# Performance work log

Hardware: AMD Instinct MI355X
Metric: run time of the kernel (lower is better)

The kernel has to match this reference:

```python
import jax, jax.numpy as jnp
import numpy as np

P = 2            # power (even positive int)
TEMPERATURE = 1.0
SCALE = 1.0 / np.sqrt(64.0)  # sqrt(head_dim) scaling
EPS = 1e-6


def setup_inputs() -> dict:
    key = jax.random.key(0)
    kq, kk, kv = jax.random.split(key, 3)
    shape = (4, 16, 2048, 64)  # (B, H, N, head_dim)
    return {
        "q": jax.random.normal(kq, shape, dtype=jnp.float32),
        "k": jax.random.normal(kk, shape, dtype=jnp.float32),
        "v": jax.random.normal(kv, shape, dtype=jnp.float32),
    }


def reference(q, k, v):
    # logits = q @ k^T * scale / temperature : (B, H, N, N)
    logits = jnp.einsum("bhnd,bhmd->bhnm", q, k) * (SCALE / TEMPERATURE)
    attn = logits ** P
    attn = attn / (attn.sum(axis=-1, keepdims=True) + EPS)
    return jnp.einsum("bhnm,bhmd->bhnd", attn, v)
```

## Files before the change

### kernel.cpp

```cpp
#include <hip/hip_runtime.h>

#define N_CTX 2048
#define DHEAD 64
#define SCALE_F 0.125f
#define EPS_F 1e-6f
#define KT 64
#define NITER (N_CTX / KT)
#define QBLK 256

typedef __attribute__((ext_vector_type(8))) short short8;
typedef __attribute__((ext_vector_type(4))) short short4v;
typedef __attribute__((ext_vector_type(4))) float float4v;
typedef __attribute__((ext_vector_type(2))) unsigned uint2v;
typedef __attribute__((ext_vector_type(4))) unsigned uint4v;

#if defined(__HIP_DEVICE_COMPILE__) && __has_builtin(__builtin_amdgcn_cvt_pk_bf16_f32)
typedef __attribute__((ext_vector_type(2))) __bf16 bf16x2;
__device__ __forceinline__ unsigned pack2(float a, float b) {
    union { bf16x2 v; unsigned u; } x;
    x.v = __builtin_amdgcn_cvt_pk_bf16_f32(a, b);
    return x.u;
}
#else
__device__ __forceinline__ unsigned bf1(float f) {
    union { float f; unsigned u; } x; x.f = f;
    return (x.u + 0x7FFFu + ((x.u >> 16) & 1u)) >> 16;
}
__device__ __forceinline__ unsigned pack2(float a, float b) {
    return bf1(a) | (bf1(b) << 16);
}
#endif

#if defined(__HIP_DEVICE_COMPILE__)
  #if __has_builtin(__builtin_amdgcn_mfma_f32_16x16x16bf16_1k)
    #define MFMA16(a, b, c) __builtin_amdgcn_mfma_f32_16x16x16bf16_1k(a, b, c, 0, 0, 0)
  #elif __has_builtin(__builtin_amdgcn_mfma_f32_16x16x16_bf16_1k)
    #define MFMA16(a, b, c) __builtin_amdgcn_mfma_f32_16x16x16_bf16_1k(a, b, c, 0, 0, 0)
  #else
    __device__ __forceinline__ float4v mfma16_asm(short4v a, short4v b, float4v c) {
        asm volatile("v_mfma_f32_16x16x16_bf16 %0, %1, %2, %0"
                     : "+v"(c) : "v"(a), "v"(b));
        return c;
    }
    #define MFMA16(a, b, c) mfma16_asm(a, b, c)
  #endif
#else
  #define MFMA16(a, b, c) (c)
#endif


__global__ __launch_bounds__(256, 2)
void powsm_attn(const float* __restrict__ qg, const float* __restrict__ kg,
                const float* __restrict__ vg, float* __restrict__ og)
{
    __shared__ short Ks[64][72];
    __shared__ short Vt[64][68];
    __shared__ float Dn[4][64];

    const int bh   = blockIdx.y;
    const int tid  = threadIdx.x;
    const int wave = tid >> 6;
    const int lane = tid & 63;
    const int qd   = lane >> 4;
    const int c    = lane & 15;

    const size_t base = (size_t)bh * N_CTX * DHEAD;
    const float* qp = qg + base;
    const float* kp = kg + base;
    const float* vp = vg + base;
    float*       op = og + base;

    const int qw0 = blockIdx.x * QBLK + wave * 64;

    short8 Qf[4][2];
    #pragma unroll
    for (int qt = 0; qt < 4; ++qt) {
        #pragma unroll
        for (int ks = 0; ks < 2; ++ks) {
            const float* src = qp + (size_t)(qw0 + qt*16 + c) * DHEAD + ks*32 + qd*8;
            float4v a = *(const float4v*)(src);
            float4v b = *(const float4v*)(src + 4);
            uint4v u;
            u[0] = pack2(a[0]*SCALE_F, a[1]*SCALE_F);
            u[1] = pack2(a[2]*SCALE_F, a[3]*SCALE_F);
            u[2] = pack2(b[0]*SCALE_F, b[1]*SCALE_F);
            u[3] = pack2(b[2]*SCALE_F, b[3]*SCALE_F);
            union { uint4v u; short8 s; } cv; cv.u = u;
            Qf[qt][ks] = cv.s;
        }
    }

    float4v Oacc[4][4];
    #pragma unroll
    for (int qt = 0; qt < 4; ++qt)
        #pragma unroll
        for (int nt = 0; nt < 4; ++nt)
            Oacc[qt][nt] = (float4v){0.f, 0.f, 0.f, 0.f};
    float4v dacc[4];
    #pragma unroll
    for (int qt = 0; qt < 4; ++qt) dacc[qt] = (float4v){0.f, 0.f, 0.f, 0.f};

    const int kr = tid >> 4;
    const int kc = tid & 15;

    float4v pK[4], pV[4];
    #pragma unroll
    for (int u = 0; u < 4; ++u)
        pK[u] = *(const float4v*)(kp + (size_t)(kr + u*16) * DHEAD + kc*4);
    #pragma unroll
    for (int j = 0; j < 4; ++j)
        pV[j] = *(const float4v*)(vp + (size_t)(4*kr + j) * DHEAD + kc*4);

    #pragma unroll 1
    for (int kvi = 0; kvi < NITER; ++kvi) {
        __syncthreads();

        #pragma unroll
        for (int u = 0; u < 4; ++u) {
            uint2v w; w[0] = pack2(pK[u][0], pK[u][1]); w[1] = pack2(pK[u][2], pK[u][3]);
            *(uint2v*)&Ks[kr + u*16][kc*4] = w;
        }
        #pragma unroll
        for (int kk = 0; kk < 4; ++kk) {
            uint2v w; w[0] = pack2(pV[0][kk], pV[1][kk]); w[1] = pack2(pV[2][kk], pV[3][kk]);
            *(uint2v*)&Vt[4*kc + kk][4*kr] = w;
        }
        __syncthreads();

        if (kvi + 1 < NITER) {
            const float* kn = kp + (size_t)(kvi + 1) * KT * DHEAD;
            const float* vn = vp + (size_t)(kvi + 1) * KT * DHEAD;
            #pragma unroll
            for (int u = 0; u < 4; ++u)
                pK[u] = *(const float4v*)(kn + (size_t)(kr + u*16) * DHEAD + kc*4);
            #pragma unroll
            for (int j = 0; j < 4; ++j)
                pV[j] = *(const float4v*)(vn + (size_t)(4*kr + j) * DHEAD + kc*4);
        }

        #pragma unroll
        for (int mt = 0; mt < 4; ++mt) {
            float4v s[4];
            #pragma unroll
            for (int qt = 0; qt < 4; ++qt) s[qt] = (float4v){0.f, 0.f, 0.f, 0.f};
            #pragma unroll
            for (int ks = 0; ks < 2; ++ks) {
                short8 af = *(const short8*)&Ks[mt*16 + c][ks*32 + qd*8];
                #pragma unroll
                for (int qt = 0; qt < 4; ++qt)
                    s[qt] = __builtin_amdgcn_mfma_f32_16x16x32_bf16(af, Qf[qt][ks], s[qt], 0, 0, 0);
            }
            short4v pa[4];
            #pragma unroll
            for (int qt = 0; qt < 4; ++qt) {
                float p0 = s[qt][0]*s[qt][0], p1 = s[qt][1]*s[qt][1];
                float p2 = s[qt][2]*s[qt][2], p3 = s[qt][3]*s[qt][3];
                dacc[qt][0] += p0; dacc[qt][1] += p1;
                dacc[qt][2] += p2; dacc[qt][3] += p3;
                union { uint2v u; short4v s; } cv;
                cv.u[0] = pack2(p0, p1); cv.u[1] = pack2(p2, p3);
                pa[qt] = cv.s;
            }
            #pragma unroll
            for (int nt = 0; nt < 4; ++nt) {
                short4v bf = *(const short4v*)&Vt[nt*16 + c][mt*16 + qd*4];
                #pragma unroll
                for (int qt = 0; qt < 4; ++qt)
                    Oacc[qt][nt] = MFMA16(pa[qt], bf, Oacc[qt][nt]);
            }
        }
    }

    #pragma unroll
    for (int qt = 0; qt < 4; ++qt) {
        float d = (dacc[qt][0] + dacc[qt][1]) + (dacc[qt][2] + dacc[qt][3]);
        d += __shfl_xor(d, 16);
        d += __shfl_xor(d, 32);
        if (qd == 0) Dn[wave][qt*16 + c] = d;
    }
    __syncthreads();

    #pragma unroll
    for (int qt = 0; qt < 4; ++qt) {
        #pragma unroll
        for (int r = 0; r < 4; ++r) {
            float inv = 1.0f / (Dn[wave][qt*16 + qd*4 + r] + EPS_F);
            float* dst = op + (size_t)(qw0 + qt*16 + qd*4 + r) * DHEAD + c;
            #pragma unroll
            for (int nt = 0; nt < 4; ++nt)
                dst[nt*16] = Oacc[qt][nt][r] * inv;
        }
    }
}

extern "C" void kernel_launch(void* const* d_in, const int* in_sizes, int n_in,
                              void* d_out, int out_size, void* d_ws, size_t ws_size,
                              hipStream_t stream) {
    const float* q = (const float*)d_in[0];
    const float* k = (const float*)d_in[1];
    const float* v = (const float*)d_in[2];
    float* out = (float*)d_out;
    dim3 grid(N_CTX / QBLK, 64, 1);
    powsm_attn<<<grid, dim3(256, 1, 1), 0, stream>>>(q, k, v, out);
}
```

Before: 209.2 us.

## Use 512-thread blocks with 32 query rows per wave and split K/V staging

Each block now runs 8 waves that each own 32 query rows instead of 4 waves owning 64, so the block still covers 256 queries. Half the waves stage K and the other half stage transposed V, which halves per-thread prefetch registers. The grid is flattened to 1D with a block-index remap that spreads (batch, head) pairs, likely for cache or XCD locality. Per-wave register use drops and occupancy should rise, but each K/V LDS fragment now feeds fewer MFMAs, so LDS reads per unit of compute double.

```diff
diff --git a/kernel.cpp b/kernel.cpp
--- a/kernel.cpp
+++ b/kernel.cpp
@@ -49,15 +49,18 @@
 #endif
 
 
-__global__ __launch_bounds__(256, 2)
+__global__ __launch_bounds__(512, 4)
 void powsm_attn(const float* __restrict__ qg, const float* __restrict__ kg,
                 const float* __restrict__ vg, float* __restrict__ og)
 {
     __shared__ short Ks[64][72];
     __shared__ short Vt[64][68];
-    __shared__ float Dn[4][64];
-
-    const int bh   = blockIdx.y;
+    __shared__ float Dn[8][32];
+
+    const int i     = blockIdx.x;
+    const int bh    = (i & 7) * 8 + ((i >> 3) & 7);
+    const int qtile = i >> 6;
+
     const int tid  = threadIdx.x;
     const int wave = tid >> 6;
     const int lane = tid & 63;
@@ -70,11 +73,11 @@
     const float* vp = vg + base;
     float*       op = og + base;
 
-    const int qw0 = blockIdx.x * QBLK + wave * 64;
-
-    short8 Qf[4][2];
-    #pragma unroll
-    for (int qt = 0; qt < 4; ++qt) {
+    const int qw0 = qtile * QBLK + wave * 32;
+
+    short8 Qf[2][2];
+    #pragma unroll
+    for (int qt = 0; qt < 2; ++qt) {
         #pragma unroll
         for (int ks = 0; ks < 2; ++ks) {
             const float* src = qp + (size_t)(qw0 + qt*16 + c) * DHEAD + ks*32 + qd*8;
@@ -90,89 +93,97 @@
         }
     }
 
-    float4v Oacc[4][4];
-    #pragma unroll
-    for (int qt = 0; qt < 4; ++qt)
+    float4v Oacc[2][4];
+    #pragma unroll
+    for (int qt = 0; qt < 2; ++qt)
         #pragma unroll
         for (int nt = 0; nt < 4; ++nt)
             Oacc[qt][nt] = (float4v){0.f, 0.f, 0.f, 0.f};
-    float4v dacc[4];
-    #pragma unroll
-    for (int qt = 0; qt < 4; ++qt) dacc[qt] = (float4v){0.f, 0.f, 0.f, 0.f};
-
-    const int kr = tid >> 4;
-    const int kc = tid & 15;
-
-    float4v pK[4], pV[4];
-    #pragma unroll
-    for (int u = 0; u < 4; ++u)
-        pK[u] = *(const float4v*)(kp + (size_t)(kr + u*16) * DHEAD + kc*4);
-    #pragma unroll
-    for (int j = 0; j < 4; ++j)
-        pV[j] = *(const float4v*)(vp + (size_t)(4*kr + j) * DHEAD + kc*4);
+    float4v dacc[2];
+    dacc[0] = (float4v){0.f, 0.f, 0.f, 0.f};
+    dacc[1] = (float4v){0.f, 0.f, 0.f, 0.f};
+
+    const bool isV = (wave >= 4);
+    const int  st  = tid & 255;
+    const int  sr  = st >> 4;
+    const int  sc  = st & 15;
+
+    float4v pf[4];
+    if (!isV) {
+        #pragma unroll
+        for (int u = 0; u < 4; ++u)
+            pf[u] = *(const float4v*)(kp + (size_t)(sr + u*16) * DHEAD + sc*4);
+    } else {
+        #pragma unroll
+        for (int j = 0; j < 4; ++j)
+            pf[j] = *(const float4v*)(vp + (size_t)(4*sr + j) * DHEAD + sc*4);
+    }
 
     #pragma unroll 1
     for (int kvi = 0; kvi < NITER; ++kvi) {
         __syncthreads();
 
-        #pragma unroll
-        for (int u = 0; u < 4; ++u) {
-            uint2v w; w[0] = pack2(pK[u][0], pK[u][1]); w[1] = pack2(pK[u][2], pK[u][3]);
-            *(uint2v*)&Ks[kr + u*16][kc*4] = w;
-        }
-        #pragma unroll
-        for (int kk = 0; kk < 4; ++kk) {
-            uint2v w; w[0] = pack2(pV[0][kk], pV[1][kk]); w[1] = pack2(pV[2][kk], pV[3][kk]);
-            *(uint2v*)&Vt[4*kc + kk][4*kr] = w;
+        if (!isV) {
+            #pragma unroll
+            for (int u = 0; u < 4; ++u) {
+                uint2v w; w[0] = pack2(pf[u][0], pf[u][1]); w[1] = pack2(pf[u][2], pf[u][3]);
+                *(uint2v*)&Ks[sr + u*16][sc*4] = w;
+            }
+        } else {
+            #pragma unroll
+            for (int kk = 0; kk < 4; ++kk) {
+                uint2v w; w[0] = pack2(pf[0][kk], pf[1][kk]); w[1] = pack2(pf[2][kk], pf[3][kk]);
+                *(uint2v*)&Vt[4*sc + kk][4*sr] = w;
+            }
         }
         __syncthreads();
 
         if (kvi + 1 < NITER) {
-            const float* kn = kp + (size_t)(kvi + 1) * KT * DHEAD;
-            const float* vn = vp + (size_t)(kvi + 1) * KT * DHEAD;
-            #pragma unroll
-            for (int u = 0; u < 4; ++u)
-                pK[u] = *(const float4v*)(kn + (size_t)(kr + u*16) * DHEAD + kc*4);
-            #pragma unroll
-            for (int j = 0; j < 4; ++j)
-                pV[j] = *(const float4v*)(vn + (size_t)(4*kr + j) * DHEAD + kc*4);
+            const float* src = (isV ? vp : kp) + (size_t)(kvi + 1) * KT * DHEAD;
+            if (!isV) {
+                #pragma unroll
+                for (int u = 0; u < 4; ++u)
+                    pf[u] = *(const float4v*)(src + (size_t)(sr + u*16) * DHEAD + sc*4);
+            } else {
+                #pragma unroll
+                for (int j = 0; j < 4; ++j)
+                    pf[j] = *(const float4v*)(src + (size_t)(4*sr + j) * DHEAD + sc*4);
+            }
         }
 
         #pragma unroll
         for (int mt = 0; mt < 4; ++mt) {
-            float4v s[4];
-            #pragma unroll
-            for (int qt = 0; qt < 4; ++qt) s[qt] = (float4v){0.f, 0.f, 0.f, 0.f};
+            float4v s[2];
+            s[0] = (float4v){0.f, 0.f, 0.f, 0.f};
+            s[1] = (float4v){0.f, 0.f, 0.f, 0.f};
             #pragma unroll
             for (int ks = 0; ks < 2; ++ks) {
                 short8 af = *(const short8*)&Ks[mt*16 + c][ks*32 + qd*8];
                 #pragma unroll
-                for (int qt = 0; qt < 4; ++qt)
+                for (int qt = 0; qt < 2; ++qt)
                     s[qt] = __builtin_amdgcn_mfma_f32_16x16x32_bf16(af, Qf[qt][ks], s[qt], 0, 0, 0);
             }
-            short4v pa[4];
-            #pragma unroll
-            for (int qt = 0; qt < 4; ++qt) {
-                float p0 = s[qt][0]*s[qt][0], p1 = s[qt][1]*s[qt][1];
-                float p2 = s[qt][2]*s[qt][2], p3 = s[qt][3]*s[qt][3];
-                dacc[qt][0] += p0; dacc[qt][1] += p1;
-                dacc[qt][2] += p2; dacc[qt][3] += p3;
+            short4v pa[2];
+            #pragma unroll
+            for (int qt = 0; qt < 2; ++qt) {
+                float4v p = s[qt] * s[qt];
+                dacc[qt] += p;
                 union { uint2v u; short4v s; } cv;
-                cv.u[0] = pack2(p0, p1); cv.u[1] = pack2(p2, p3);
+                cv.u[0] = pack2(p[0], p[1]); cv.u[1] = pack2(p[2], p[3]);
                 pa[qt] = cv.s;
             }
             #pragma unroll
             for (int nt = 0; nt < 4; ++nt) {
                 short4v bf = *(const short4v*)&Vt[nt*16 + c][mt*16 + qd*4];
                 #pragma unroll
-                for (int qt = 0; qt < 4; ++qt)
+                for (int qt = 0; qt < 2; ++qt)
                     Oacc[qt][nt] = MFMA16(pa[qt], bf, Oacc[qt][nt]);
             }
         }
     }
 
     #pragma unroll
-    for (int qt = 0; qt < 4; ++qt) {
+    for (int qt = 0; qt < 2; ++qt) {
         float d = (dacc[qt][0] + dacc[qt][1]) + (dacc[qt][2] + dacc[qt][3]);
         d += __shfl_xor(d, 16);
         d += __shfl_xor(d, 32);
@@ -181,7 +192,7 @@
     __syncthreads();
 
     #pragma unroll
-    for (int qt = 0; qt < 4; ++qt) {
+    for (int qt = 0; qt < 2; ++qt) {
         #pragma unroll
         for (int r = 0; r < 4; ++r) {
             float inv = 1.0f / (Dn[wave][qt*16 + qd*4 + r] + EPS_F);
@@ -200,6 +211,6 @@
     const float* k = (const float*)d_in[1];
     const float* v = (const float*)d_in[2];
     float* out = (float*)d_out;
-    dim3 grid(N_CTX / QBLK, 64, 1);
-    powsm_attn<<<grid, dim3(256, 1, 1), 0, stream>>>(q, k, v, out);
-}
+    dim3 grid((N_CTX / QBLK) * 64, 1, 1);
+    powsm_attn<<<grid, dim3(512, 1, 1), 0, stream>>>(q, k, v, out);
+}
```

After: 210.9 us. About the same (+0.8%).
